# Kernel tuning notes

Hardware: AMD Instinct MI355X
Metric: run time of the kernel (lower is better)

## Reference

```python
import jax, jax.numpy as jnp
import numpy as np

TRANSCRIBER_WEIGHT = 1.0
PREDICTOR_WEIGHT = 1.0


def setup_inputs() -> dict:
    key = jax.random.key(0)
    k1, k2, k3, k4 = jax.random.split(key, 4)
    B, T, U, D, V = 8, 256, 64, 512, 1024
    x = jax.random.normal(k1, (B, T, D), dtype=jnp.float32)   # transcriber output
    y = jax.random.normal(k2, (B, U, D), dtype=jnp.float32)   # predictor output
    # nn.Linear(D, V): weight [V, D], bias [V]
    W = jax.random.normal(k3, (V, D), dtype=jnp.float32) * (1.0 / np.sqrt(D))
    b = jax.random.normal(k4, (V,), dtype=jnp.float32) * 0.01
    return {"x": x, "y": y, "W": W, "b": b}


def reference(x, y, W, b):
    # h: [B, T, U, D] = tw * x[:, :, None, :] + pw * y[:, None, :, :]
    h = TRANSCRIBER_WEIGHT * x[:, :, None, :] + PREDICTOR_WEIGHT * y[:, None, :, :]
    h = jax.nn.relu(h)
    # linear: [B, T, U, V]
    return jnp.einsum('btud,vd->btuv', h, W) + b
```

## Files before the change

### kernel.cpp

```cpp
#include <hip/hip_runtime.h>
#include <hip/hip_bf16.h>


constexpr int Bc = 8, Tc = 256, Uc = 64, Dc = 512, Vc = 1024;
constexpr int BM = 64, BN = 512;
constexpr int NSTEPS = 16;
constexpr int BDIM = 512;

typedef __attribute__((ext_vector_type(8)))  short short8;
typedef __attribute__((ext_vector_type(8)))  unsigned short ushort8;
typedef __attribute__((ext_vector_type(4)))  float f32x4;
typedef __attribute__((ext_vector_type(16))) float f32x16;

__device__ inline unsigned short f2bf(float f) {
    union { float f; unsigned u; } v; v.f = f;
    unsigned r = v.u + 0x7FFFu + ((v.u >> 16) & 1u);
    return (unsigned short)(r >> 16);
}

__global__ __launch_bounds__(256) void cvt_wt(const float* __restrict__ W,
                                              unsigned short* __restrict__ Wt) {
    const int idx  = blockIdx.x * 256 + threadIdx.x;
    const int v    = idx >> 6;
    const int koct = idx & 63;
    const float4 a = *(const float4*)(W + (size_t)v * Dc + koct * 8);
    const float4 b = *(const float4*)(W + (size_t)v * Dc + koct * 8 + 4);
    ushort8 o;
    o[0] = f2bf(a.x); o[1] = f2bf(a.y); o[2] = f2bf(a.z); o[3] = f2bf(a.w);
    o[4] = f2bf(b.x); o[5] = f2bf(b.y); o[6] = f2bf(b.z); o[7] = f2bf(b.w);
    const size_t chunk = (size_t)(koct >> 1) * 2048 + v * 2 + (koct & 1);
    *(ushort8*)(Wt + chunk * 8) = o;
}

__global__ __launch_bounds__(BDIM, 4) void joiner_v6(
    const float* __restrict__ x, const float* __restrict__ y,
    const unsigned short* __restrict__ Wt, const float* __restrict__ bias,
    float* __restrict__ out)
{
    __shared__ __align__(16) unsigned char smem[BM * Dc * 2];
    unsigned short* As = (unsigned short*)smem;

    const int tid  = threadIdx.x;
    const int lane = tid & 63;
    const int wid  = tid >> 6;
    const int l31  = lane & 31;
    const int l32  = lane >> 5;

    const int nhalf = blockIdx.x & 1;
    const int mb    = blockIdx.x >> 1;
    const int bb    = mb >> 8;
    const int tt    = mb & 255;
    const int m0    = mb * BM;
    const int n0    = nhalf * BN;
    const int colbase = n0 + wid * 64;

    float bv[2];
    bv[0] = bias[colbase + l31];
    bv[1] = bias[colbase + 32 + l31];

    const float* xrow = x + (size_t)(bb * Tc + tt) * Dc;
    #pragma unroll
    for (int i = 0; i < 8; ++i) {
        const int c = tid + i * BDIM;
        const int u = c >> 6;
        const int s = c & 63;
        const float4* xp = (const float4*)(xrow + s * 8);
        const float4* yp = (const float4*)(y + ((size_t)(bb * Uc + u) * Dc + s * 8));
        float4 xa = xp[0], xb = xp[1];
        float4 ya = yp[0], yb = yp[1];
        ushort8 hv;
        hv[0] = f2bf(fmaxf(xa.x + ya.x, 0.f));
        hv[1] = f2bf(fmaxf(xa.y + ya.y, 0.f));
        hv[2] = f2bf(fmaxf(xa.z + ya.z, 0.f));
        hv[3] = f2bf(fmaxf(xa.w + ya.w, 0.f));
        hv[4] = f2bf(fmaxf(xb.x + yb.x, 0.f));
        hv[5] = f2bf(fmaxf(xb.y + yb.y, 0.f));
        hv[6] = f2bf(fmaxf(xb.z + yb.z, 0.f));
        hv[7] = f2bf(fmaxf(xb.w + yb.w, 0.f));
        *(ushort8*)(&As[u * Dc + ((s ^ (u & 7)) * 8)]) = hv;
    }
    __syncthreads();

    const unsigned short* pW = Wt + (size_t)(colbase * 2 + 2 * l31 + l32) * 8;

    f32x16 acc[2][2] = {};
    short8 wfA[2][2], wfB[2][2];

    #define LOADW(buf, ks)                                                    \
        {                                                                     \
            _Pragma("unroll")                                                 \
            for (int q = 0; q < 2; ++q)                                       \
                _Pragma("unroll")                                             \
                for (int n16 = 0; n16 < 2; ++n16)                             \
                    buf[q][n16] = *(const short8*)(pW + ((ks) * 2 + q) * 16384 \
                                                   + n16 * 512);              \
        }

    #define STEP(cur, nxt, ks)                                                \
        {                                                                     \
            if ((ks) + 1 < NSTEPS) LOADW(nxt, (ks) + 1);                      \
            _Pragma("unroll")                                                 \
            for (int q = 0; q < 2; ++q) {                                     \
                const int oA = (ks) * 4 + q * 2 + l32;                        \
                short8 af0 = *(const short8*)(&As[l31 * Dc                    \
                                              + ((oA ^ (l31 & 7)) * 8)]);     \
                short8 af1 = *(const short8*)(&As[(32 + l31) * Dc             \
                                              + ((oA ^ (l31 & 7)) * 8)]);     \
                __builtin_amdgcn_s_setprio(1);                                \
                acc[0][0] = __builtin_amdgcn_mfma_f32_32x32x16_bf16(          \
                    af0, cur[q][0], acc[0][0], 0, 0, 0);                      \
                acc[0][1] = __builtin_amdgcn_mfma_f32_32x32x16_bf16(          \
                    af0, cur[q][1], acc[0][1], 0, 0, 0);                      \
                acc[1][0] = __builtin_amdgcn_mfma_f32_32x32x16_bf16(          \
                    af1, cur[q][0], acc[1][0], 0, 0, 0);                      \
                acc[1][1] = __builtin_amdgcn_mfma_f32_32x32x16_bf16(          \
                    af1, cur[q][1], acc[1][1], 0, 0, 0);                      \
                __builtin_amdgcn_s_setprio(0);                                \
            }                                                                 \
        }

    LOADW(wfA, 0);
    #pragma unroll
    for (int ks = 0; ks < NSTEPS; ks += 2) {
        STEP(wfA, wfB, ks);
        STEP(wfB, wfA, ks + 1);
    }
    #undef STEP
    #undef LOADW

    __syncthreads();
    float* tr = (float*)smem + wid * (16 * 36);
    #pragma unroll
    for (int m16 = 0; m16 < 2; ++m16) {
        #pragma unroll
        for (int n16 = 0; n16 < 2; ++n16) {
            #pragma unroll
            for (int h = 0; h < 2; ++h) {
                #pragma unroll
                for (int e = 0; e < 8; ++e) {
                    const int rl = (e & 3) + 8 * (e >> 2) + 4 * l32;
                    tr[rl * 36 + l31] = acc[m16][n16][h * 8 + e] + bv[n16];
                }
                #pragma unroll
                for (int h2 = 0; h2 < 2; ++h2) {
                    const int rr = h2 * 8 + (lane >> 3);
                    const int c4 = (lane & 7) * 4;
                    f32x4 o;
                    o[0] = tr[rr * 36 + c4 + 0];
                    o[1] = tr[rr * 36 + c4 + 1];
                    o[2] = tr[rr * 36 + c4 + 2];
                    o[3] = tr[rr * 36 + c4 + 3];
                    const size_t off =
                        (size_t)(m0 + m16 * 32 + h * 16 + rr) * Vc
                        + colbase + n16 * 32 + c4;
                    __builtin_nontemporal_store(o, (f32x4*)(out + off));
                }
            }
        }
    }
}

constexpr int F_BM = 128, F_BN = 128, F_BK = 64;
constexpr int F_MT = (Bc * Tc * Uc) / F_BM;
constexpr int F_NT = Vc / F_BN;

__global__ __launch_bounds__(256) void joiner_mfma(
    const float* __restrict__ x, const float* __restrict__ y,
    const float* __restrict__ W, const float* __restrict__ bias,
    float* __restrict__ out)
{
    __shared__ unsigned short As[F_BM * F_BK];
    __shared__ unsigned short Wsh[F_BN * F_BK];
    const int tid = threadIdx.x;
    const int mtile = blockIdx.x % F_MT;
    const int ntile = blockIdx.x / F_MT;
    const int m0 = mtile * F_BM, v0 = ntile * F_BN;
    const int bb = m0 / (Tc * Uc);
    const int t0 = (m0 % (Tc * Uc)) / Uc;
    const int lane = tid & 63, wid = tid >> 6;
    const int wm = wid >> 1, wn = wid & 1;
    const int lr = lane & 15, lk8 = lane >> 4;
    f32x4 acc[4][4] = {};
    for (int k0 = 0; k0 < Dc; k0 += F_BK) {
        __syncthreads();
        #pragma unroll
        for (int i = 0; i < 4; ++i) {
            const int chunk = tid + i * 256;
            const int row = chunk >> 3, slot = chunk & 7;
            const int ps8 = (slot ^ (row & 7)) * 8;
            const int t = t0 + (row >> 6), u = row & 63;
            const float4* xp = (const float4*)(x + ((size_t)(bb * Tc + t) * Dc + k0 + slot * 8));
            const float4* yp = (const float4*)(y + ((size_t)(bb * Uc + u) * Dc + k0 + slot * 8));
            float4 xa = xp[0], xb2 = xp[1], ya = yp[0], yb2 = yp[1];
            ushort8 hv;
            hv[0] = f2bf(fmaxf(xa.x + ya.x, 0.f)); hv[1] = f2bf(fmaxf(xa.y + ya.y, 0.f));
            hv[2] = f2bf(fmaxf(xa.z + ya.z, 0.f)); hv[3] = f2bf(fmaxf(xa.w + ya.w, 0.f));
            hv[4] = f2bf(fmaxf(xb2.x + yb2.x, 0.f)); hv[5] = f2bf(fmaxf(xb2.y + yb2.y, 0.f));
            hv[6] = f2bf(fmaxf(xb2.z + yb2.z, 0.f)); hv[7] = f2bf(fmaxf(xb2.w + yb2.w, 0.f));
            *(ushort8*)(&As[row * F_BK + ps8]) = hv;
            const float4* wp = (const float4*)(W + ((size_t)(v0 + row) * Dc + k0 + slot * 8));
            float4 wa = wp[0], wb2 = wp[1];
            ushort8 wv;
            wv[0] = f2bf(wa.x); wv[1] = f2bf(wa.y); wv[2] = f2bf(wa.z); wv[3] = f2bf(wa.w);
            wv[4] = f2bf(wb2.x); wv[5] = f2bf(wb2.y); wv[6] = f2bf(wb2.z); wv[7] = f2bf(wb2.w);
            *(ushort8*)(&Wsh[row * F_BK + ps8]) = wv;
        }
        __syncthreads();
        #pragma unroll
        for (int kk = 0; kk < 2; ++kk) {
            const int psk = kk * 4 + lk8;
            short8 af[4], bfr[4];
            #pragma unroll
            for (int mf = 0; mf < 4; ++mf) {
                const int row = wm * 64 + mf * 16 + lr;
                af[mf] = *(const short8*)(&As[row * F_BK + ((psk ^ (row & 7)) * 8)]);
            }
            #pragma unroll
            for (int nf = 0; nf < 4; ++nf) {
                const int row = wn * 64 + nf * 16 + lr;
                bfr[nf] = *(const short8*)(&Wsh[row * F_BK + ((psk ^ (row & 7)) * 8)]);
            }
            #pragma unroll
            for (int mf = 0; mf < 4; ++mf)
                #pragma unroll
                for (int nf = 0; nf < 4; ++nf)
                    acc[mf][nf] = __builtin_amdgcn_mfma_f32_16x16x32_bf16(af[mf], bfr[nf], acc[mf][nf], 0, 0, 0);
        }
    }
    #pragma unroll
    for (int nf = 0; nf < 4; ++nf) {
        const int v = v0 + wn * 64 + nf * 16 + lr;
        const float bv = bias[v];
        #pragma unroll
        for (int mf = 0; mf < 4; ++mf) {
            const int mrow = m0 + wm * 64 + mf * 16 + (lane >> 4) * 4;
            #pragma unroll
            for (int j = 0; j < 4; ++j)
                out[(size_t)(mrow + j) * Vc + v] = acc[mf][nf][j] + bv;
        }
    }
}

extern "C" void kernel_launch(void* const* d_in, const int* in_sizes, int n_in,
                              void* d_out, int out_size, void* d_ws, size_t ws_size,
                              hipStream_t stream) {
    const float* x = (const float*)d_in[0];
    const float* y = (const float*)d_in[1];
    const float* W = (const float*)d_in[2];
    const float* b = (const float*)d_in[3];
    float* out = (float*)d_out;

    const size_t w_bytes = (size_t)Vc * Dc * sizeof(unsigned short);
    if (ws_size >= w_bytes) {
        unsigned short* Wt = (unsigned short*)d_ws;
        cvt_wt<<<dim3((Vc * Dc / 8) / 256), 256, 0, stream>>>(W, Wt);
        joiner_v6<<<dim3((Bc * Tc * Uc / BM) * (Vc / BN)), BDIM, 0, stream>>>(x, y, Wt, b, out);
    } else {
        joiner_mfma<<<dim3(F_MT * F_NT), 256, 0, stream>>>(x, y, W, b, out);
    }
}
```

Measured before the change: 201.5 us.

## Double M tile to 128 rows so each W fragment feeds more MFMAs

Doubles the block's M tile from 64 to 128 rows, covering two consecutive time steps. Each wave now runs 4x2 MFMA accumulators per loaded weight fragment, which halves weight traffic per output and halves the grid size. LDS rises to 128 KB per block and occupancy drops to 2 blocks per CU, with more accumulator registers and fewer blocks to hide latency.

```diff
diff --git a/kernel.cpp b/kernel.cpp
--- a/kernel.cpp
+++ b/kernel.cpp
@@ -3,7 +3,7 @@
 
 
 constexpr int Bc = 8, Tc = 256, Uc = 64, Dc = 512, Vc = 1024;
-constexpr int BM = 64, BN = 512;
+constexpr int BM = 128, BN = 512;
 constexpr int NSTEPS = 16;
 constexpr int BDIM = 512;
 
@@ -32,7 +32,7 @@
     *(ushort8*)(Wt + chunk * 8) = o;
 }
 
-__global__ __launch_bounds__(BDIM, 4) void joiner_v6(
+__global__ __launch_bounds__(BDIM, 2) void joiner_v7(
     const float* __restrict__ x, const float* __restrict__ y,
     const unsigned short* __restrict__ Wt, const float* __restrict__ bias,
     float* __restrict__ out)
@@ -48,8 +48,8 @@
 
     const int nhalf = blockIdx.x & 1;
     const int mb    = blockIdx.x >> 1;
-    const int bb    = mb >> 8;
-    const int tt    = mb & 255;
+    const int bb    = mb >> 7;
+    const int t0    = (mb & 127) * 2;
     const int m0    = mb * BM;
     const int n0    = nhalf * BN;
     const int colbase = n0 + wid * 64;
@@ -58,14 +58,14 @@
     bv[0] = bias[colbase + l31];
     bv[1] = bias[colbase + 32 + l31];
 
-    const float* xrow = x + (size_t)(bb * Tc + tt) * Dc;
-    #pragma unroll
-    for (int i = 0; i < 8; ++i) {
+    const float* xrow0 = x + (size_t)(bb * Tc + t0) * Dc;
+    #pragma unroll
+    for (int i = 0; i < 16; ++i) {
         const int c = tid + i * BDIM;
-        const int u = c >> 6;
+        const int r = c >> 6;
         const int s = c & 63;
-        const float4* xp = (const float4*)(xrow + s * 8);
-        const float4* yp = (const float4*)(y + ((size_t)(bb * Uc + u) * Dc + s * 8));
+        const float4* xp = (const float4*)(xrow0 + (size_t)(r >> 6) * Dc + s * 8);
+        const float4* yp = (const float4*)(y + ((size_t)(bb * Uc + (r & 63)) * Dc + s * 8));
         float4 xa = xp[0], xb = xp[1];
         float4 ya = yp[0], yb = yp[1];
         ushort8 hv;
@@ -77,13 +77,13 @@
         hv[5] = f2bf(fmaxf(xb.y + yb.y, 0.f));
         hv[6] = f2bf(fmaxf(xb.z + yb.z, 0.f));
         hv[7] = f2bf(fmaxf(xb.w + yb.w, 0.f));
-        *(ushort8*)(&As[u * Dc + ((s ^ (u & 7)) * 8)]) = hv;
+        *(ushort8*)(&As[r * Dc + ((s ^ (r & 7)) * 8)]) = hv;
     }
     __syncthreads();
 
     const unsigned short* pW = Wt + (size_t)(colbase * 2 + 2 * l31 + l32) * 8;
 
-    f32x16 acc[2][2] = {};
+    f32x16 acc[4][2] = {};
     short8 wfA[2][2], wfB[2][2];
 
     #define LOADW(buf, ks)                                                    \
@@ -102,19 +102,19 @@
             _Pragma("unroll")                                                 \
             for (int q = 0; q < 2; ++q) {                                     \
                 const int oA = (ks) * 4 + q * 2 + l32;                        \
-                short8 af0 = *(const short8*)(&As[l31 * Dc                    \
-                                              + ((oA ^ (l31 & 7)) * 8)]);     \
-                short8 af1 = *(const short8*)(&As[(32 + l31) * Dc             \
-                                              + ((oA ^ (l31 & 7)) * 8)]);     \
+                short8 af[4];                                                 \
+                _Pragma("unroll")                                             \
+                for (int m16 = 0; m16 < 4; ++m16)                             \
+                    af[m16] = *(const short8*)(&As[(m16 * 32 + l31) * Dc      \
+                                               + ((oA ^ (l31 & 7)) * 8)]);    \
                 __builtin_amdgcn_s_setprio(1);                                \
-                acc[0][0] = __builtin_amdgcn_mfma_f32_32x32x16_bf16(          \
-                    af0, cur[q][0], acc[0][0], 0, 0, 0);                      \
-                acc[0][1] = __builtin_amdgcn_mfma_f32_32x32x16_bf16(          \
-                    af0, cur[q][1], acc[0][1], 0, 0, 0);                      \
-                acc[1][0] = __builtin_amdgcn_mfma_f32_32x32x16_bf16(          \
-                    af1, cur[q][0], acc[1][0], 0, 0, 0);                      \
-                acc[1][1] = __builtin_amdgcn_mfma_f32_32x32x16_bf16(          \
-                    af1, cur[q][1], acc[1][1], 0, 0, 0);                      \
+                _Pragma("unroll")                                             \
+                for (int m16 = 0; m16 < 4; ++m16) {                           \
+                    acc[m16][0] = __builtin_amdgcn_mfma_f32_32x32x16_bf16(    \
+                        af[m16], cur[q][0], acc[m16][0], 0, 0, 0);            \
+                    acc[m16][1] = __builtin_amdgcn_mfma_f32_32x32x16_bf16(    \
+                        af[m16], cur[q][1], acc[m16][1], 0, 0, 0);            \
+                }                                                             \
                 __builtin_amdgcn_s_setprio(0);                                \
             }                                                                 \
         }
@@ -131,7 +131,7 @@
     __syncthreads();
     float* tr = (float*)smem + wid * (16 * 36);
     #pragma unroll
-    for (int m16 = 0; m16 < 2; ++m16) {
+    for (int m16 = 0; m16 < 4; ++m16) {
         #pragma unroll
         for (int n16 = 0; n16 < 2; ++n16) {
             #pragma unroll
@@ -254,7 +254,7 @@
     if (ws_size >= w_bytes) {
         unsigned short* Wt = (unsigned short*)d_ws;
         cvt_wt<<<dim3((Vc * Dc / 8) / 256), 256, 0, stream>>>(W, Wt);
-        joiner_v6<<<dim3((Bc * Tc * Uc / BM) * (Vc / BN)), BDIM, 0, stream>>>(x, y, Wt, b, out);
+        joiner_v7<<<dim3((Bc * Tc * Uc / BM) * (Vc / BN)), BDIM, 0, stream>>>(x, y, Wt, b, out);
     } else {
         joiner_mfma<<<dim3(F_MT * F_NT), 256, 0, stream>>>(x, y, W, b, out);
     }
```

After: 241.7 us. 19.9% more time.
